# Performance work log

Measured on AMD Instinct MI355X. Metric: run time of the kernel, lower is better.

Reference implementation:

```python
import jax, jax.numpy as jnp
import numpy as np

STRIDES = (8, 16, 32)
C = 80          # num_classes
KA = 3          # anchors per level
TOPK = 100      # per-level top-k
CONF_TH = 0.001
NMS_TH = 0.5
INPUT_SIZE = 2048
ANCHOR_SIZES = np.array([[[10, 13], [16, 30], [33, 23]],
                         [[30, 61], [62, 45], [59, 119]],
                         [[116, 90], [156, 198], [373, 326]]], dtype=np.float32)


def make_anchors(level):
    # Mirrors YOLOv3.create_grid: torch.meshgrid default is 'ij' indexing.
    fmp = INPUT_SIZE // STRIDES[level]
    gy, gx = np.meshgrid(np.arange(fmp), np.arange(fmp), indexing='ij')
    grid_xy = np.stack([gx, gy], axis=-1).reshape(-1, 1, 2).astype(np.float32)  # [HW,1,2]
    grid_xy = np.broadcast_to(grid_xy, (fmp * fmp, KA, 2))
    wh = np.broadcast_to(ANCHOR_SIZES[level][None], (fmp * fmp, KA, 2))
    return jnp.asarray(np.concatenate([grid_xy, wh], axis=-1).reshape(-1, 4))  # [HW*KA,4]


def setup_inputs() -> dict:
    key = jax.random.key(0)
    ks = jax.random.split(key, 9)
    d = {}
    for lvl in range(3):
        N = (INPUT_SIZE // STRIDES[lvl]) ** 2 * KA
        d[f"conf_pred_{lvl + 1}"] = jax.random.normal(ks[3 * lvl], (N, 1), jnp.float32)
        d[f"cls_pred_{lvl + 1}"] = jax.random.normal(ks[3 * lvl + 1], (N, C), jnp.float32)
        d[f"reg_pred_{lvl + 1}"] = jax.random.normal(ks[3 * lvl + 2], (N, 4), jnp.float32) * 0.5
        d[f"anchors_{lvl + 1}"] = make_anchors(lvl)
    return d


def _level(conf, cls, reg, anchors, stride):
    # scores = sigmoid(objectness) * softmax(class logits), flattened over (anchor, class)
    prob = jax.nn.sigmoid(conf) * jax.nn.softmax(cls, axis=-1)      # [N,C]
    scores, idx = jax.lax.top_k(prob.reshape(-1), TOPK)             # [TOPK]
    valid = scores > CONF_TH
    a_idx = idx // C
    labels = idx % C
    r = reg[a_idx]                                                  # [TOPK,4]
    a = anchors[a_idx]                                              # [TOPK,4]
    # decode_boxes: xy = (sigmoid(txy)+grid)*stride ; wh = exp(twh)*anchor_wh
    xy = (jax.nn.sigmoid(r[:, :2]) + a[:, :2]) * stride
    wh = jnp.exp(r[:, 2:]) * a[:, 2:]
    boxes = jnp.concatenate([xy - 0.5 * wh, xy + 0.5 * wh], axis=-1)  # x1y1x2y2
    return scores, labels, boxes, valid


def reference(conf_pred_1, cls_pred_1, reg_pred_1,
              conf_pred_2, cls_pred_2, reg_pred_2,
              conf_pred_3, cls_pred_3, reg_pred_3,
              anchors_1, anchors_2, anchors_3):
    levels = [(conf_pred_1, cls_pred_1, reg_pred_1, anchors_1, STRIDES[0]),
              (conf_pred_2, cls_pred_2, reg_pred_2, anchors_2, STRIDES[1]),
              (conf_pred_3, cls_pred_3, reg_pred_3, anchors_3, STRIDES[2])]
    parts = [_level(*lv) for lv in levels]
    scores = jnp.concatenate([p[0] for p in parts])   # [3*TOPK]
    labels = jnp.concatenate([p[1] for p in parts])
    boxes = jnp.concatenate([p[2] for p in parts], axis=0)
    valid = jnp.concatenate([p[3] for p in parts])

    # Sort all candidates by score descending (greedy NMS order)
    order = jnp.argsort(-scores)
    scores, labels, boxes, valid = scores[order], labels[order], boxes[order], valid[order]

    x1, y1, x2, y2 = boxes[:, 0], boxes[:, 1], boxes[:, 2], boxes[:, 3]
    areas = (x2 - x1) * (y2 - y1)
    xx1 = jnp.maximum(x1[:, None], x1[None, :])
    yy1 = jnp.maximum(y1[:, None], y1[None, :])
    xx2 = jnp.minimum(x2[:, None], x2[None, :])
    yy2 = jnp.minimum(y2[:, None], y2[None, :])
    w = jnp.maximum(1e-10, xx2 - xx1)
    h = jnp.maximum(1e-10, yy2 - yy1)
    inter = w * h
    iou = inter / (areas[:, None] + areas[None, :] - inter)

    K = scores.shape[0]
    idxr = jnp.arange(K)
    # class-wise suppression: only same-label, lower-scored boxes can be suppressed
    sup_cond = (iou > NMS_TH) & (labels[:, None] == labels[None, :]) & (idxr[None, :] > idxr[:, None])

    def body(i, keep):
        return keep & ~(sup_cond[i] & keep[i])

    keep = jax.lax.fori_loop(0, K, body, valid)

    boxes_n = jnp.clip(boxes / INPUT_SIZE, 0.0, 1.0)
    out = jnp.concatenate([boxes_n, scores[:, None], labels.astype(jnp.float32)[:, None]], axis=1)
    return jnp.where(keep[:, None], out, 0.0)   # [3*TOPK, 6] = (x1,y1,x2,y2,score,label)
```

## Files before the change

### kernel.cpp

```cpp
#include <hip/hip_runtime.h>
#include <math.h>
#include <stdint.h>

#define NBUCKET 4096
#define NCOPY   8
#define CAP     16384
#define QCAP    4096
#define STAGE   4096
#define FCAP    1024
#define TOPK    100
#define NLVL    3
#define NCLS    80

#define PA_G1 1024
#define PA_G2 256
#define PA_G3 64
#define CK_G1 192
#define CK_G2 48
#define CK_G3 12

__global__ void zero_kernel(uint4* __restrict__ p)
{
    p[blockIdx.x * 256 + threadIdx.x] = make_uint4(0u, 0u, 0u, 0u);
}

__global__ void passA_kernel(const float* __restrict__ conf1, const float* __restrict__ cls1,
                             const float* __restrict__ conf2, const float* __restrict__ cls2,
                             const float* __restrict__ conf3, const float* __restrict__ cls3,
                             int n1, int n2, int n3,
                             unsigned int* __restrict__ ghist,
                             float* __restrict__ amax)
{
    const float* conf; const float* cls; int nA, nb, b;
    unsigned int* gh; float* am;
    if (blockIdx.x < PA_G1) {
        b = blockIdx.x; conf = conf1; cls = cls1; nA = n1; nb = PA_G1;
        gh = ghist; am = amax;
    } else if (blockIdx.x < PA_G1 + PA_G2) {
        b = blockIdx.x - PA_G1; conf = conf2; cls = cls2; nA = n2; nb = PA_G2;
        gh = ghist + NCOPY * NBUCKET; am = amax + n1;
    } else {
        b = blockIdx.x - PA_G1 - PA_G2; conf = conf3; cls = cls3; nA = n3; nb = PA_G3;
        gh = ghist + 2 * NCOPY * NBUCKET; am = amax + n1 + n2;
    }

    __shared__ unsigned int sh[NBUCKET];
    for (int i = threadIdx.x; i < NBUCKET; i += 256) sh[i] = 0;
    __syncthreads();

    int sub = threadIdx.x & 15;
    int g16 = threadIdx.x >> 4;
    int nChunk = nA >> 4;
    for (int ch = b; ch < nChunk; ch += nb) {
        int a = (ch << 4) + g16;
        float cv  = conf[a];
        float sig = 1.0f / (1.0f + expf(-cv));
        const float* row = cls + (size_t)a * NCLS + sub;
        float c0 = row[0], c1 = row[16], c2 = row[32], c3 = row[48], c4 = row[64];
        float m = fmaxf(fmaxf(fmaxf(c0, c1), fmaxf(c2, c3)), c4);
#pragma unroll
        for (int o = 8; o >= 1; o >>= 1) m = fmaxf(m, __shfl_xor(m, o, 16));
        float s = ((expf(c0 - m) + expf(c1 - m)) + (expf(c2 - m) + expf(c3 - m))) + expf(c4 - m);
#pragma unroll
        for (int o = 8; o >= 1; o >>= 1) s += __shfl_xor(s, o, 16);
        float inv = sig / s;
        if (sub == 0) {
            am[a] = inv;
            unsigned bk = __float_as_uint(inv) >> 18;
            if (bk > NBUCKET - 1) bk = NBUCKET - 1;
            atomicAdd(&sh[bk], 1u);
        }
    }
    __syncthreads();
    unsigned int* g = gh + (b & (NCOPY - 1)) * NBUCKET;
    for (int i = threadIdx.x; i < NBUCKET; i += 256) {
        unsigned v = sh[i];
        if (v) atomicAdd(&g[i], v);
    }
}

__global__ void scan_kernel(const unsigned int* __restrict__ ghist,
                            unsigned int* __restrict__ thresh,
                            unsigned int* __restrict__ ccount)
{
    int lvl = blockIdx.x;
    const unsigned int* h0 = ghist + lvl * NCOPY * NBUCKET;
    __shared__ unsigned int h[NBUCKET];
    __shared__ unsigned int ps[256];
    int t = threadIdx.x;
    if (t == 0) ccount[lvl] = 0;
    for (int bb = t; bb < NBUCKET; bb += 256) {
        unsigned s = 0;
        for (int c = 0; c < NCOPY; c++) s += h0[c * NBUCKET + bb];
        h[bb] = s;
    }
    __syncthreads();
    unsigned cs = 0;
#pragma unroll
    for (int i = 0; i < 16; i++) cs += h[NBUCKET - 1 - (t * 16 + i)];
    ps[t] = cs;
    __syncthreads();
    for (int o = 1; o < 256; o <<= 1) {
        unsigned v = (t >= o) ? ps[t - o] : 0u;
        __syncthreads();
        ps[t] += v;
        __syncthreads();
    }
    unsigned incl = ps[t], excl = incl - cs;
    if (excl < TOPK && incl >= TOPK) {
        unsigned cum = excl, B = 0;
        for (int i = 0; i < 16; i++) {
            int bb = NBUCKET - 1 - (t * 16 + i);
            cum += h[bb];
            if (cum >= TOPK) { B = (unsigned)bb; break; }
        }
        thresh[lvl] = B << 18;
    }
}

__global__ void compact_kernel(const float* __restrict__ conf1, const float* __restrict__ cls1,
                               const float* __restrict__ conf2, const float* __restrict__ cls2,
                               const float* __restrict__ conf3, const float* __restrict__ cls3,
                               int n1, int n2, int n3,
                               const unsigned int* __restrict__ thresh,
                               const float* __restrict__ amax,
                               unsigned int* __restrict__ ccount,
                               float* __restrict__ cscore,
                               unsigned int* __restrict__ cidx)
{
    const float* conf; const float* cls; int bl, lvl; const float* am;
    if (blockIdx.x < CK_G1)              { lvl = 0; bl = blockIdx.x;               conf = conf1; cls = cls1; am = amax; }
    else if (blockIdx.x < CK_G1 + CK_G2) { lvl = 1; bl = blockIdx.x - CK_G1;       conf = conf2; cls = cls2; am = amax + n1; }
    else                                 { lvl = 2; bl = blockIdx.x - CK_G1 - CK_G2; conf = conf3; cls = cls3; am = amax + n1 + n2; }

    __shared__ int qn;
    __shared__ int queue[QCAP];
    if (threadIdx.x == 0) qn = 0;
    __syncthreads();

    unsigned T = thresh[lvl];
    int idx4 = bl * 256 + threadIdx.x;
    const float4* am4 = (const float4*)am;
    float4 v = am4[idx4];
    float vv[4] = {v.x, v.y, v.z, v.w};
#pragma unroll
    for (int j = 0; j < 4; j++) {
        if (__float_as_uint(vv[j]) >= T) {
            int p = atomicAdd(&qn, 1);
            if (p < QCAP) queue[p] = idx4 * 4 + j;
        }
    }
    __syncthreads();
    int qcnt = min(qn, QCAP);
    int grp = threadIdx.x >> 4;
    int sub = threadIdx.x & 15;
    float*        csl = cscore + lvl * CAP;
    unsigned int* cil = cidx   + lvl * CAP;
    for (int q = grp; q < qcnt; q += 16) {
        int a = queue[q];
        float cv  = conf[a];
        float sig = 1.0f / (1.0f + expf(-cv));
        const float* row = cls + (size_t)a * NCLS + sub;
        float c0 = row[0], c1 = row[16], c2 = row[32], c3 = row[48], c4 = row[64];
        float m = fmaxf(fmaxf(fmaxf(c0, c1), fmaxf(c2, c3)), c4);
#pragma unroll
        for (int o = 8; o >= 1; o >>= 1) m = fmaxf(m, __shfl_xor(m, o, 16));
        float e0 = expf(c0 - m), e1 = expf(c1 - m), e2 = expf(c2 - m),
              e3 = expf(c3 - m), e4 = expf(c4 - m);
        float s = ((e0 + e1) + (e2 + e3)) + e4;
#pragma unroll
        for (int o = 8; o >= 1; o >>= 1) s += __shfl_xor(s, o, 16);
        float inv = sig / s;
        float e[5] = {e0, e1, e2, e3, e4};
#pragma unroll
        for (int k = 0; k < 5; k++) {
            float p = e[k] * inv;
            if (e[k] == 1.0f || __float_as_uint(p) >= T) {
                unsigned pos = atomicAdd(&ccount[lvl], 1u);
                if (pos < CAP) {
                    csl[pos] = p;
                    cil[pos] = (unsigned)(a * NCLS + sub + 16 * k);
                }
            }
        }
    }
}

__global__ __launch_bounds__(1024, 4) void select_kernel(
    const float* __restrict__ cscore, const unsigned int* __restrict__ cidx,
    const unsigned int* __restrict__ ccount,
    const unsigned int* __restrict__ thresh,
    float* __restrict__ sel_sc, int* __restrict__ sel_ix)
{
    int lvl = blockIdx.x;
    int tid = threadIdx.x;
    __shared__ float        q_sc[STAGE];
    __shared__ unsigned int q_ix[STAGE];
    __shared__ unsigned int subh[4096];
    __shared__ unsigned int ps[1024];
    __shared__ unsigned int kthr_s;
    __shared__ int          fcnt;
    __shared__ float        f_sc[FCAP];
    __shared__ unsigned int f_ix[FCAP];

    int cnt = min((int)ccount[lvl], CAP);
    const float*        sc = cscore + lvl * CAP;
    const unsigned int* ix = cidx   + lvl * CAP;
    int n = min(cnt, STAGE);
    unsigned B12 = (thresh[lvl] >> 18) << 12;

    for (int i = tid; i < 4096; i += 1024) subh[i] = 0;
    if (tid == 0) fcnt = 0;
    for (int c = tid; c < n; c += 1024) { q_sc[c] = sc[c]; q_ix[c] = ix[c]; }
    if (tid < TOPK) { sel_sc[lvl * TOPK + tid] = -1e30f; sel_ix[lvl * TOPK + tid] = 0; }
    __syncthreads();

    for (int c = tid; c < cnt; c += 1024) {
        float v = (c < n) ? q_sc[c] : sc[c];
        unsigned rel = (__float_as_uint(v) >> 6) - B12;
        if (rel > 4095u) rel = 4095u;
        atomicAdd(&subh[rel], 1u);
    }
    __syncthreads();

    unsigned cs = 0;
#pragma unroll
    for (int i = 0; i < 4; i++) cs += subh[4095 - 4 * tid - i];
    ps[tid] = cs;
    __syncthreads();
    for (int o = 1; o < 1024; o <<= 1) {
        unsigned v = (tid >= o) ? ps[tid - o] : 0u;
        __syncthreads();
        ps[tid] += v;
        __syncthreads();
    }
    {
        unsigned incl = ps[tid], excl = incl - cs;
        if (excl < TOPK && incl >= TOPK) {
            unsigned cum = excl;
            for (int i = 0; i < 4; i++) {
                int sb = 4095 - 4 * tid - i;
                cum += subh[sb];
                if (cum >= TOPK) { kthr_s = (B12 + (unsigned)sb) << 6; break; }
            }
        }
    }
    __syncthreads();
    unsigned kthr = kthr_s;

    for (int c = tid; c < cnt; c += 1024) {
        float v; unsigned vi;
        if (c < n) { v = q_sc[c]; vi = q_ix[c]; }
        else       { v = sc[c];   vi = ix[c];   }
        if (__float_as_uint(v) >= kthr) {
            int p = atomicAdd(&fcnt, 1);
            if (p < FCAP) { f_sc[p] = v; f_ix[p] = vi; }
        }
    }
    __syncthreads();
    int fn = min(fcnt, FCAP);

    for (int c = tid; c < fn; c += 1024) {
        float    my  = f_sc[c];
        unsigned myi = f_ix[c];
        int rank = 0;
        for (int k = 0; k < fn; k++) {
            float v = f_sc[k];
            rank += (v > my) || (v == my && f_ix[k] < myi);
        }
        if (rank < TOPK) {
            sel_sc[lvl * TOPK + rank] = my;
            sel_ix[lvl * TOPK + rank] = (int)myi;
        }
    }
}

__device__ __forceinline__ float rlf(float x, int l)
{
    return __uint_as_float((unsigned)__builtin_amdgcn_readlane((int)__float_as_uint(x), l));
}
__device__ __forceinline__ int rli(int x, int l)
{
    return __builtin_amdgcn_readlane(x, l);
}
__device__ __forceinline__ unsigned long long rl64(unsigned long long x, int b)
{
    unsigned lo = (unsigned)__builtin_amdgcn_readlane((int)(unsigned)x, b);
    unsigned hi = (unsigned)__builtin_amdgcn_readlane((int)(unsigned)(x >> 32), b);
    return ((unsigned long long)hi << 32) | lo;
}

__global__ void prep_kernel(
    const float* __restrict__ reg1, const float* __restrict__ anch1,
    const float* __restrict__ reg2, const float* __restrict__ anch2,
    const float* __restrict__ reg3, const float* __restrict__ anch3,
    const float* __restrict__ sel_sc, const int* __restrict__ sel_ix,
    float* __restrict__ t_score, float* __restrict__ t_box,
    int* __restrict__ t_label, int* __restrict__ t_valid)
{
    int tid  = threadIdx.x;
    int lane = tid & 63;

    float sg[5];
#pragma unroll
    for (int g = 0; g < 5; g++) {
        int k = g * 64 + lane;
        sg[g] = (k < 300) ? sel_sc[k] : -INFINITY;
    }

    float my = (tid < 300) ? sel_sc[tid] : -INFINITY;
    int rank = 0;
#pragma unroll
    for (int g = 0; g < 5; g++) {
        int base = g * 64;
#pragma unroll 1
        for (int ii = 0; ii < 64; ii++) {
            float v = rlf(sg[g], ii);
            int k = base + ii;
            rank += (v > my) || (v == my && k < tid);
        }
    }

    if (tid < 300) {
        int lvl = tid / TOPK;
        const float* reg = lvl == 0 ? reg1 : (lvl == 1 ? reg2 : reg3);
        const float* anc = lvl == 0 ? anch1 : (lvl == 1 ? anch2 : anch3);
        float stride = lvl == 0 ? 8.0f : (lvl == 1 ? 16.0f : 32.0f);
        int  idx = sel_ix[tid];
        int a   = idx / NCLS;
        int lab = idx % NCLS;
        float r0 = reg[4 * a + 0], r1 = reg[4 * a + 1], r2 = reg[4 * a + 2], r3 = reg[4 * a + 3];
        float a0 = anc[4 * a + 0], a1 = anc[4 * a + 1], a2 = anc[4 * a + 2], a3 = anc[4 * a + 3];
        float cx = (1.0f / (1.0f + expf(-r0)) + a0) * stride;
        float cy = (1.0f / (1.0f + expf(-r1)) + a1) * stride;
        float w  = expf(r2) * a2;
        float h  = expf(r3) * a3;
        t_score[rank]       = my;
        t_box[4 * rank + 0] = cx - 0.5f * w;
        t_box[4 * rank + 1] = cy - 0.5f * h;
        t_box[4 * rank + 2] = cx + 0.5f * w;
        t_box[4 * rank + 3] = cy + 0.5f * h;
        t_label[rank] = lab;
        t_valid[rank] = my > 0.001f;
    }
}

__global__ void sup_kernel(const float* __restrict__ t_box,
                           const int* __restrict__ t_label,
                           unsigned long long* __restrict__ sup_ws)
{
    int tid  = threadIdx.x;
    int lane = tid & 63;
    int w    = tid >> 6;
    int rbase = 20 * blockIdx.x;

    float bx1 = 0, by1 = 0, bx2 = 0, by2 = 0, areaj = 0;
    int labj = -1;
    if (tid < 300) {
        bx1 = t_box[4 * tid + 0]; by1 = t_box[4 * tid + 1];
        bx2 = t_box[4 * tid + 2]; by2 = t_box[4 * tid + 3];
        labj = t_label[tid];
        areaj = (bx2 - bx1) * (by2 - by1);
    }

    float rx1 = 0, ry1 = 0, rx2 = 0, ry2 = 0, rar = 1.0f;
    int rlab = -9;
    int r = rbase + lane;
    if (lane < 20 && r < 300) {
        rx1 = t_box[4 * r + 0]; ry1 = t_box[4 * r + 1];
        rx2 = t_box[4 * r + 2]; ry2 = t_box[4 * r + 3];
        rar = (rx2 - rx1) * (ry2 - ry1);
        rlab = t_label[r];
    }

#pragma unroll 1
    for (int ii = 0; ii < 20; ii++) {
        int i = rbase + ii;
        float xi1 = rlf(rx1, ii), yi1 = rlf(ry1, ii);
        float xi2 = rlf(rx2, ii), yi2 = rlf(ry2, ii);
        float ari = rlf(rar, ii);
        int  labi = rli(rlab, ii);
        float xx1 = fmaxf(xi1, bx1), yy1 = fmaxf(yi1, by1);
        float xx2 = fminf(xi2, bx2), yy2 = fminf(yi2, by2);
        float ww = fmaxf(1e-10f, xx2 - xx1);
        float hh = fmaxf(1e-10f, yy2 - yy1);
        float inter = ww * hh;
        float iou = inter / (ari + areaj - inter);
        bool p = (tid > i) && (labj == labi) && (iou > 0.5f) && (tid < 300);
        unsigned long long m = __ballot(p);
        if (lane == 0) sup_ws[i * 5 + w] = m;
    }
}

__global__ void nmsfin_kernel(const float* __restrict__ t_score,
                              const float* __restrict__ t_box,
                              const int* __restrict__ t_label,
                              const int* __restrict__ t_valid,
                              const unsigned long long* __restrict__ sup_ws,
                              float* __restrict__ out)
{
    int lane = threadIdx.x;

    unsigned long long s0[5], s1[5], s2[5], s3[5], s4[5];
#pragma unroll
    for (int q = 0; q < 5; q++) {
        s0[q] = sup_ws[(lane)       * 5 + q];
        s1[q] = sup_ws[(lane + 64)  * 5 + q];
        s2[q] = sup_ws[(lane + 128) * 5 + q];
        s3[q] = sup_ws[(lane + 192) * 5 + q];
        s4[q] = (lane + 256 < 300) ? sup_ws[(lane + 256) * 5 + q] : 0ull;
    }

    unsigned long long k0 = __ballot(t_valid[lane] != 0);
    unsigned long long k1 = __ballot(t_valid[lane + 64] != 0);
    unsigned long long k2 = __ballot(t_valid[lane + 128] != 0);
    unsigned long long k3 = __ballot(t_valid[lane + 192] != 0);
    unsigned long long k4 = __ballot((lane + 256 < 300) ? (t_valid[lane + 256] != 0) : false);

    unsigned long long nz0 = __ballot((s0[0] | s0[1] | s0[2] | s0[3] | s0[4]) != 0ull);
    unsigned long long nz1 = __ballot((s1[0] | s1[1] | s1[2] | s1[3] | s1[4]) != 0ull);
    unsigned long long nz2 = __ballot((s2[0] | s2[1] | s2[2] | s2[3] | s2[4]) != 0ull);
    unsigned long long nz3 = __ballot((s3[0] | s3[1] | s3[2] | s3[3] | s3[4]) != 0ull);
    unsigned long long nz4 = __ballot((s4[0] | s4[1] | s4[2] | s4[3] | s4[4]) != 0ull);

#define NMS_SPARSE(SR, KR, NZ)                                                \
    {                                                                         \
        unsigned long long m = (NZ);                                          \
        while (m) {                                                           \
            int b = __builtin_ctzll(m);                                       \
            m &= m - 1ull;                                                    \
            if ((KR >> b) & 1ull) {                                           \
                k0 &= ~rl64(SR[0], b);                                        \
                k1 &= ~rl64(SR[1], b);                                        \
                k2 &= ~rl64(SR[2], b);                                        \
                k3 &= ~rl64(SR[3], b);                                        \
                k4 &= ~rl64(SR[4], b);                                        \
            }                                                                 \
        }                                                                     \
    }
    NMS_SPARSE(s0, k0, nz0)
    NMS_SPARSE(s1, k1, nz1)
    NMS_SPARSE(s2, k2, nz2)
    NMS_SPARSE(s3, k3, nz3)
    NMS_SPARSE(s4, k4, nz4)
#undef NMS_SPARSE

#pragma unroll 1
    for (int e = lane; e < 300 * 6; e += 64) {
        int row = e / 6, col = e % 6;
        unsigned long long kw = (row < 64) ? k0 : (row < 128) ? k1 : (row < 192) ? k2
                              : (row < 256) ? k3 : k4;
        bool kept = (kw >> (row & 63)) & 1ull;
        float v = 0.0f;
        if (kept) {
            if (col < 4) {
                v = t_box[4 * row + col] * (1.0f / 2048.0f);
                v = fminf(fmaxf(v, 0.0f), 1.0f);
            } else if (col == 4) {
                v = t_score[row];
            } else {
                v = (float)t_label[row];
            }
        }
        out[e] = v;
    }
}

extern "C" void kernel_launch(void* const* d_in, const int* in_sizes, int n_in,
                              void* d_out, int out_size, void* d_ws, size_t ws_size,
                              hipStream_t stream)
{
    const float* conf1 = (const float*)d_in[0];
    const float* cls1  = (const float*)d_in[1];
    const float* reg1  = (const float*)d_in[2];
    const float* anch1 = (const float*)d_in[3];
    const float* conf2 = (const float*)d_in[4];
    const float* cls2  = (const float*)d_in[5];
    const float* reg2  = (const float*)d_in[6];
    const float* anch2 = (const float*)d_in[7];
    const float* conf3 = (const float*)d_in[8];
    const float* cls3  = (const float*)d_in[9];
    const float* reg3  = (const float*)d_in[10];
    const float* anch3 = (const float*)d_in[11];

    int N1 = in_sizes[0];
    int N2 = in_sizes[4];
    int N3 = in_sizes[8];

    unsigned int* wsu    = (unsigned int*)d_ws;
    unsigned int* hist   = wsu;
    unsigned int* thresh = wsu + NLVL * NCOPY * NBUCKET;
    unsigned int* ccount = thresh + NLVL;
    float*        amax   = (float*)(wsu + NLVL * NCOPY * NBUCKET + 16);
    float*        cscore = amax + (N1 + N2 + N3);
    unsigned int* cidx   = (unsigned int*)(cscore + NLVL * CAP);
    float*        sel_sc = (float*)(cidx + NLVL * CAP);
    int*          sel_ix = (int*)(sel_sc + NLVL * TOPK);
    float*        t_score = (float*)(sel_ix + NLVL * TOPK);
    float*        t_box   = t_score + 300;
    int*          t_label = (int*)(t_box + 1200);
    int*          t_valid = t_label + 300;
    unsigned long long* sup_ws =
        (unsigned long long*)(((uintptr_t)(t_valid + 300) + 15) & ~(uintptr_t)15);

    zero_kernel<<<96, 256, 0, stream>>>((uint4*)hist);

    passA_kernel<<<PA_G1 + PA_G2 + PA_G3, 256, 0, stream>>>(
        conf1, cls1, conf2, cls2, conf3, cls3, N1, N2, N3, hist, amax);

    scan_kernel<<<NLVL, 256, 0, stream>>>(hist, thresh, ccount);

    compact_kernel<<<CK_G1 + CK_G2 + CK_G3, 256, 0, stream>>>(
        conf1, cls1, conf2, cls2, conf3, cls3, N1, N2, N3,
        thresh, amax, ccount, cscore, cidx);

    select_kernel<<<NLVL, 1024, 0, stream>>>(cscore, cidx, ccount, thresh, sel_sc, sel_ix);

    prep_kernel<<<1, 320, 0, stream>>>(reg1, anch1, reg2, anch2, reg3, anch3,
                                       sel_sc, sel_ix, t_score, t_box, t_label, t_valid);

    sup_kernel<<<15, 320, 0, stream>>>(t_box, t_label, sup_ws);

    nmsfin_kernel<<<1, 64, 0, stream>>>(t_score, t_box, t_label, t_valid, sup_ws, (float*)d_out);
}
```

Baseline: 92.55 us.

## Fuse tail kernels via last-block-done counters and unroll passA two chunks per iteration

Merges select with prep, and sup with the NMS finalize, into two kernels. Each uses an atomic completion counter so that the last block to finish runs the follow-on stage, which removes two kernel launches and their inter-kernel gaps. The select block size drops from 1024 to 320 threads, and the block-wide prefix scan becomes a single-wavefront shuffle scan over 64-bucket groups. passA now processes two chunks per loop iteration to get more loads in flight. The counters are zeroed in zero_kernel, which adds threadfence and atomic synchronisation overhead, and fewer threads now share the select work.

```diff
diff --git a/kernel.cpp b/kernel.cpp
--- a/kernel.cpp
+++ b/kernel.cpp
@@ -19,9 +19,10 @@
 #define CK_G2 48
 #define CK_G3 12
 
-__global__ void zero_kernel(uint4* __restrict__ p)
+__global__ void zero_kernel(uint4* __restrict__ p, unsigned int* __restrict__ ctr)
 {
     p[blockIdx.x * 256 + threadIdx.x] = make_uint4(0u, 0u, 0u, 0u);
+    if (blockIdx.x == 0 && threadIdx.x == 0) { ctr[0] = 0u; ctr[1] = 0u; }
 }
 
 __global__ void passA_kernel(const float* __restrict__ conf1, const float* __restrict__ cls1,
@@ -51,24 +52,52 @@
     int sub = threadIdx.x & 15;
     int g16 = threadIdx.x >> 4;
     int nChunk = nA >> 4;
-    for (int ch = b; ch < nChunk; ch += nb) {
-        int a = (ch << 4) + g16;
-        float cv  = conf[a];
-        float sig = 1.0f / (1.0f + expf(-cv));
-        const float* row = cls + (size_t)a * NCLS + sub;
-        float c0 = row[0], c1 = row[16], c2 = row[32], c3 = row[48], c4 = row[64];
-        float m = fmaxf(fmaxf(fmaxf(c0, c1), fmaxf(c2, c3)), c4);
-#pragma unroll
-        for (int o = 8; o >= 1; o >>= 1) m = fmaxf(m, __shfl_xor(m, o, 16));
-        float s = ((expf(c0 - m) + expf(c1 - m)) + (expf(c2 - m) + expf(c3 - m))) + expf(c4 - m);
-#pragma unroll
-        for (int o = 8; o >= 1; o >>= 1) s += __shfl_xor(s, o, 16);
-        float inv = sig / s;
-        if (sub == 0) {
-            am[a] = inv;
-            unsigned bk = __float_as_uint(inv) >> 18;
-            if (bk > NBUCKET - 1) bk = NBUCKET - 1;
-            atomicAdd(&sh[bk], 1u);
+    for (int ch = b; ch < nChunk; ch += 2 * nb) {
+        int a0 = (ch << 4) + g16;
+        int ch1 = ch + nb;
+        bool has1 = ch1 < nChunk;
+        float cv0 = conf[a0];
+        const float* r0 = cls + (size_t)a0 * NCLS + sub;
+        float A0 = r0[0], A1 = r0[16], A2 = r0[32], A3 = r0[48], A4 = r0[64];
+        float cv1 = 0.0f, B0 = 0, B1 = 0, B2 = 0, B3 = 0, B4 = 0;
+        int a1 = 0;
+        if (has1) {
+            a1 = (ch1 << 4) + g16;
+            cv1 = conf[a1];
+            const float* r1 = cls + (size_t)a1 * NCLS + sub;
+            B0 = r1[0]; B1 = r1[16]; B2 = r1[32]; B3 = r1[48]; B4 = r1[64];
+        }
+        {
+            float sig = 1.0f / (1.0f + expf(-cv0));
+            float m = fmaxf(fmaxf(fmaxf(A0, A1), fmaxf(A2, A3)), A4);
+#pragma unroll
+            for (int o = 8; o >= 1; o >>= 1) m = fmaxf(m, __shfl_xor(m, o, 16));
+            float s = ((expf(A0 - m) + expf(A1 - m)) + (expf(A2 - m) + expf(A3 - m))) + expf(A4 - m);
+#pragma unroll
+            for (int o = 8; o >= 1; o >>= 1) s += __shfl_xor(s, o, 16);
+            float inv = sig / s;
+            if (sub == 0) {
+                am[a0] = inv;
+                unsigned bk = __float_as_uint(inv) >> 18;
+                if (bk > NBUCKET - 1) bk = NBUCKET - 1;
+                atomicAdd(&sh[bk], 1u);
+            }
+        }
+        if (has1) {
+            float sig = 1.0f / (1.0f + expf(-cv1));
+            float m = fmaxf(fmaxf(fmaxf(B0, B1), fmaxf(B2, B3)), B4);
+#pragma unroll
+            for (int o = 8; o >= 1; o >>= 1) m = fmaxf(m, __shfl_xor(m, o, 16));
+            float s = ((expf(B0 - m) + expf(B1 - m)) + (expf(B2 - m) + expf(B3 - m))) + expf(B4 - m);
+#pragma unroll
+            for (int o = 8; o >= 1; o >>= 1) s += __shfl_xor(s, o, 16);
+            float inv = sig / s;
+            if (sub == 0) {
+                am[a1] = inv;
+                unsigned bk = __float_as_uint(inv) >> 18;
+                if (bk > NBUCKET - 1) bk = NBUCKET - 1;
+                atomicAdd(&sh[bk], 1u);
+            }
         }
     }
     __syncthreads();
@@ -186,22 +215,43 @@
     }
 }
 
-__global__ __launch_bounds__(1024, 4) void select_kernel(
+__device__ __forceinline__ float rlf(float x, int l)
+{
+    return __uint_as_float((unsigned)__builtin_amdgcn_readlane((int)__float_as_uint(x), l));
+}
+__device__ __forceinline__ int rli(int x, int l)
+{
+    return __builtin_amdgcn_readlane(x, l);
+}
+__device__ __forceinline__ unsigned long long rl64(unsigned long long x, int b)
+{
+    unsigned lo = (unsigned)__builtin_amdgcn_readlane((int)(unsigned)x, b);
+    unsigned hi = (unsigned)__builtin_amdgcn_readlane((int)(unsigned)(x >> 32), b);
+    return ((unsigned long long)hi << 32) | lo;
+}
+
+__global__ __launch_bounds__(320) void select_prep_kernel(
     const float* __restrict__ cscore, const unsigned int* __restrict__ cidx,
     const unsigned int* __restrict__ ccount,
     const unsigned int* __restrict__ thresh,
-    float* __restrict__ sel_sc, int* __restrict__ sel_ix)
+    float* __restrict__ sel_sc, int* __restrict__ sel_ix,
+    const float* __restrict__ reg1, const float* __restrict__ anch1,
+    const float* __restrict__ reg2, const float* __restrict__ anch2,
+    const float* __restrict__ reg3, const float* __restrict__ anch3,
+    float* __restrict__ t_score, float* __restrict__ t_box,
+    int* __restrict__ t_label, int* __restrict__ t_valid,
+    unsigned int* __restrict__ sel_done)
 {
     int lvl = blockIdx.x;
     int tid = threadIdx.x;
     __shared__ float        q_sc[STAGE];
     __shared__ unsigned int q_ix[STAGE];
     __shared__ unsigned int subh[4096];
-    __shared__ unsigned int ps[1024];
     __shared__ unsigned int kthr_s;
     __shared__ int          fcnt;
     __shared__ float        f_sc[FCAP];
     __shared__ unsigned int f_ix[FCAP];
+    __shared__ int          lastflag;
 
     int cnt = min((int)ccount[lvl], CAP);
     const float*        sc = cscore + lvl * CAP;
@@ -209,13 +259,13 @@
     int n = min(cnt, STAGE);
     unsigned B12 = (thresh[lvl] >> 18) << 12;
 
-    for (int i = tid; i < 4096; i += 1024) subh[i] = 0;
+    for (int i = tid; i < 4096; i += 320) subh[i] = 0;
     if (tid == 0) fcnt = 0;
-    for (int c = tid; c < n; c += 1024) { q_sc[c] = sc[c]; q_ix[c] = ix[c]; }
+    for (int c = tid; c < n; c += 320) { q_sc[c] = sc[c]; q_ix[c] = ix[c]; }
     if (tid < TOPK) { sel_sc[lvl * TOPK + tid] = -1e30f; sel_ix[lvl * TOPK + tid] = 0; }
     __syncthreads();
 
-    for (int c = tid; c < cnt; c += 1024) {
+    for (int c = tid; c < cnt; c += 320) {
         float v = (c < n) ? q_sc[c] : sc[c];
         unsigned rel = (__float_as_uint(v) >> 6) - B12;
         if (rel > 4095u) rel = 4095u;
@@ -223,32 +273,29 @@
     }
     __syncthreads();
 
-    unsigned cs = 0;
-#pragma unroll
-    for (int i = 0; i < 4; i++) cs += subh[4095 - 4 * tid - i];
-    ps[tid] = cs;
-    __syncthreads();
-    for (int o = 1; o < 1024; o <<= 1) {
-        unsigned v = (tid >= o) ? ps[tid - o] : 0u;
-        __syncthreads();
-        ps[tid] += v;
-        __syncthreads();
-    }
-    {
-        unsigned incl = ps[tid], excl = incl - cs;
-        if (excl < TOPK && incl >= TOPK) {
+    if (tid < 64) {
+        int base = 4095 - (tid << 6);
+        unsigned csum = 0;
+        for (int i = 0; i < 64; i++) csum += subh[base - i];
+        unsigned v = csum;
+        for (int o = 1; o < 64; o <<= 1) {
+            unsigned u = __shfl_up(v, o);
+            if (tid >= o) v += u;
+        }
+        unsigned excl = v - csum;
+        if (excl < TOPK && v >= TOPK) {
             unsigned cum = excl;
-            for (int i = 0; i < 4; i++) {
-                int sb = 4095 - 4 * tid - i;
-                cum += subh[sb];
-                if (cum >= TOPK) { kthr_s = (B12 + (unsigned)sb) << 6; break; }
+            for (int i = 0; i < 64; i++) {
+                int bb = base - i;
+                cum += subh[bb];
+                if (cum >= TOPK) { kthr_s = (B12 + (unsigned)bb) << 6; break; }
             }
         }
     }
     __syncthreads();
     unsigned kthr = kthr_s;
 
-    for (int c = tid; c < cnt; c += 1024) {
+    for (int c = tid; c < cnt; c += 320) {
         float v; unsigned vi;
         if (c < n) { v = q_sc[c]; vi = q_ix[c]; }
         else       { v = sc[c];   vi = ix[c];   }
@@ -260,7 +307,7 @@
     __syncthreads();
     int fn = min(fcnt, FCAP);
 
-    for (int c = tid; c < fn; c += 1024) {
+    for (int c = tid; c < fn; c += 320) {
         float    my  = f_sc[c];
         unsigned myi = f_ix[c];
         int rank = 0;
@@ -273,86 +320,75 @@
             sel_ix[lvl * TOPK + rank] = (int)myi;
         }
     }
-}
-
-__device__ __forceinline__ float rlf(float x, int l)
-{
-    return __uint_as_float((unsigned)__builtin_amdgcn_readlane((int)__float_as_uint(x), l));
-}
-__device__ __forceinline__ int rli(int x, int l)
-{
-    return __builtin_amdgcn_readlane(x, l);
-}
-__device__ __forceinline__ unsigned long long rl64(unsigned long long x, int b)
-{
-    unsigned lo = (unsigned)__builtin_amdgcn_readlane((int)(unsigned)x, b);
-    unsigned hi = (unsigned)__builtin_amdgcn_readlane((int)(unsigned)(x >> 32), b);
-    return ((unsigned long long)hi << 32) | lo;
-}
-
-__global__ void prep_kernel(
-    const float* __restrict__ reg1, const float* __restrict__ anch1,
-    const float* __restrict__ reg2, const float* __restrict__ anch2,
-    const float* __restrict__ reg3, const float* __restrict__ anch3,
-    const float* __restrict__ sel_sc, const int* __restrict__ sel_ix,
-    float* __restrict__ t_score, float* __restrict__ t_box,
-    int* __restrict__ t_label, int* __restrict__ t_valid)
-{
-    int tid  = threadIdx.x;
-    int lane = tid & 63;
-
-    float sg[5];
-#pragma unroll
-    for (int g = 0; g < 5; g++) {
-        int k = g * 64 + lane;
-        sg[g] = (k < 300) ? sel_sc[k] : -INFINITY;
-    }
-
-    float my = (tid < 300) ? sel_sc[tid] : -INFINITY;
-    int rank = 0;
-#pragma unroll
-    for (int g = 0; g < 5; g++) {
-        int base = g * 64;
+
+    __syncthreads();
+    if (tid == 0) {
+        __threadfence();
+        unsigned prev = atomicAdd(sel_done, 1u);
+        lastflag = (prev == NLVL - 1);
+    }
+    __syncthreads();
+    if (!lastflag) return;
+    if (tid == 0) __threadfence();
+    __syncthreads();
+
+    {
+        int lane = tid & 63;
+        float sg[5];
+#pragma unroll
+        for (int g = 0; g < 5; g++) {
+            int k = g * 64 + lane;
+            sg[g] = (k < 300) ? sel_sc[k] : -INFINITY;
+        }
+        float my = (tid < 300) ? sel_sc[tid] : -INFINITY;
+        int rank = 0;
+#pragma unroll
+        for (int g = 0; g < 5; g++) {
+            int base = g * 64;
 #pragma unroll 1
-        for (int ii = 0; ii < 64; ii++) {
-            float v = rlf(sg[g], ii);
-            int k = base + ii;
-            rank += (v > my) || (v == my && k < tid);
-        }
-    }
-
-    if (tid < 300) {
-        int lvl = tid / TOPK;
-        const float* reg = lvl == 0 ? reg1 : (lvl == 1 ? reg2 : reg3);
-        const float* anc = lvl == 0 ? anch1 : (lvl == 1 ? anch2 : anch3);
-        float stride = lvl == 0 ? 8.0f : (lvl == 1 ? 16.0f : 32.0f);
-        int  idx = sel_ix[tid];
-        int a   = idx / NCLS;
-        int lab = idx % NCLS;
-        float r0 = reg[4 * a + 0], r1 = reg[4 * a + 1], r2 = reg[4 * a + 2], r3 = reg[4 * a + 3];
-        float a0 = anc[4 * a + 0], a1 = anc[4 * a + 1], a2 = anc[4 * a + 2], a3 = anc[4 * a + 3];
-        float cx = (1.0f / (1.0f + expf(-r0)) + a0) * stride;
-        float cy = (1.0f / (1.0f + expf(-r1)) + a1) * stride;
-        float w  = expf(r2) * a2;
-        float h  = expf(r3) * a3;
-        t_score[rank]       = my;
-        t_box[4 * rank + 0] = cx - 0.5f * w;
-        t_box[4 * rank + 1] = cy - 0.5f * h;
-        t_box[4 * rank + 2] = cx + 0.5f * w;
-        t_box[4 * rank + 3] = cy + 0.5f * h;
-        t_label[rank] = lab;
-        t_valid[rank] = my > 0.001f;
-    }
-}
-
-__global__ void sup_kernel(const float* __restrict__ t_box,
-                           const int* __restrict__ t_label,
-                           unsigned long long* __restrict__ sup_ws)
+            for (int ii = 0; ii < 64; ii++) {
+                float v = rlf(sg[g], ii);
+                int k = base + ii;
+                rank += (v > my) || (v == my && k < tid);
+            }
+        }
+        if (tid < 300) {
+            int lv = tid / TOPK;
+            const float* reg = lv == 0 ? reg1 : (lv == 1 ? reg2 : reg3);
+            const float* anc = lv == 0 ? anch1 : (lv == 1 ? anch2 : anch3);
+            float stride = lv == 0 ? 8.0f : (lv == 1 ? 16.0f : 32.0f);
+            int  idx = sel_ix[tid];
+            int a   = idx / NCLS;
+            int lab = idx % NCLS;
+            float r0 = reg[4 * a + 0], r1 = reg[4 * a + 1], r2 = reg[4 * a + 2], r3 = reg[4 * a + 3];
+            float a0 = anc[4 * a + 0], a1 = anc[4 * a + 1], a2 = anc[4 * a + 2], a3 = anc[4 * a + 3];
+            float cx = (1.0f / (1.0f + expf(-r0)) + a0) * stride;
+            float cy = (1.0f / (1.0f + expf(-r1)) + a1) * stride;
+            float w  = expf(r2) * a2;
+            float h  = expf(r3) * a3;
+            t_score[rank]       = my;
+            t_box[4 * rank + 0] = cx - 0.5f * w;
+            t_box[4 * rank + 1] = cy - 0.5f * h;
+            t_box[4 * rank + 2] = cx + 0.5f * w;
+            t_box[4 * rank + 3] = cy + 0.5f * h;
+            t_label[rank] = lab;
+            t_valid[rank] = my > 0.001f;
+        }
+    }
+}
+
+__global__ __launch_bounds__(320) void supnms_kernel(
+    const float* __restrict__ t_score, const float* __restrict__ t_box,
+    const int* __restrict__ t_label, const int* __restrict__ t_valid,
+    unsigned long long* __restrict__ sup_ws,
+    unsigned int* __restrict__ sup_done,
+    float* __restrict__ out)
 {
     int tid  = threadIdx.x;
     int lane = tid & 63;
     int w    = tid >> 6;
     int rbase = 20 * blockIdx.x;
+    __shared__ int lastflag;
 
     float bx1 = 0, by1 = 0, bx2 = 0, by2 = 0, areaj = 0;
     int labj = -1;
@@ -390,79 +426,82 @@
         unsigned long long m = __ballot(p);
         if (lane == 0) sup_ws[i * 5 + w] = m;
     }
-}
-
-__global__ void nmsfin_kernel(const float* __restrict__ t_score,
-                              const float* __restrict__ t_box,
-                              const int* __restrict__ t_label,
-                              const int* __restrict__ t_valid,
-                              const unsigned long long* __restrict__ sup_ws,
-                              float* __restrict__ out)
-{
-    int lane = threadIdx.x;
-
-    unsigned long long s0[5], s1[5], s2[5], s3[5], s4[5];
-#pragma unroll
-    for (int q = 0; q < 5; q++) {
-        s0[q] = sup_ws[(lane)       * 5 + q];
-        s1[q] = sup_ws[(lane + 64)  * 5 + q];
-        s2[q] = sup_ws[(lane + 128) * 5 + q];
-        s3[q] = sup_ws[(lane + 192) * 5 + q];
-        s4[q] = (lane + 256 < 300) ? sup_ws[(lane + 256) * 5 + q] : 0ull;
-    }
-
-    unsigned long long k0 = __ballot(t_valid[lane] != 0);
-    unsigned long long k1 = __ballot(t_valid[lane + 64] != 0);
-    unsigned long long k2 = __ballot(t_valid[lane + 128] != 0);
-    unsigned long long k3 = __ballot(t_valid[lane + 192] != 0);
-    unsigned long long k4 = __ballot((lane + 256 < 300) ? (t_valid[lane + 256] != 0) : false);
-
-    unsigned long long nz0 = __ballot((s0[0] | s0[1] | s0[2] | s0[3] | s0[4]) != 0ull);
-    unsigned long long nz1 = __ballot((s1[0] | s1[1] | s1[2] | s1[3] | s1[4]) != 0ull);
-    unsigned long long nz2 = __ballot((s2[0] | s2[1] | s2[2] | s2[3] | s2[4]) != 0ull);
-    unsigned long long nz3 = __ballot((s3[0] | s3[1] | s3[2] | s3[3] | s3[4]) != 0ull);
-    unsigned long long nz4 = __ballot((s4[0] | s4[1] | s4[2] | s4[3] | s4[4]) != 0ull);
+
+    __syncthreads();
+    if (tid == 0) {
+        __threadfence();
+        unsigned prev = atomicAdd(sup_done, 1u);
+        lastflag = (prev == 14);
+    }
+    __syncthreads();
+    if (!lastflag) return;
+    if (tid == 0) __threadfence();
+    __syncthreads();
+
+    if (tid < 64) {
+        unsigned long long s0[5], s1[5], s2[5], s3[5], s4[5];
+#pragma unroll
+        for (int q = 0; q < 5; q++) {
+            s0[q] = sup_ws[(lane)       * 5 + q];
+            s1[q] = sup_ws[(lane + 64)  * 5 + q];
+            s2[q] = sup_ws[(lane + 128) * 5 + q];
+            s3[q] = sup_ws[(lane + 192) * 5 + q];
+            s4[q] = (lane + 256 < 300) ? sup_ws[(lane + 256) * 5 + q] : 0ull;
+        }
+
+        unsigned long long k0 = __ballot(t_valid[lane] != 0);
+        unsigned long long k1 = __ballot(t_valid[lane + 64] != 0);
+        unsigned long long k2 = __ballot(t_valid[lane + 128] != 0);
+        unsigned long long k3 = __ballot(t_valid[lane + 192] != 0);
+        unsigned long long k4 = __ballot((lane + 256 < 300) ? (t_valid[lane + 256] != 0) : false);
+
+        unsigned long long nz0 = __ballot((s0[0] | s0[1] | s0[2] | s0[3] | s0[4]) != 0ull);
+        unsigned long long nz1 = __ballot((s1[0] | s1[1] | s1[2] | s1[3] | s1[4]) != 0ull);
+        unsigned long long nz2 = __ballot((s2[0] | s2[1] | s2[2] | s2[3] | s2[4]) != 0ull);
+        unsigned long long nz3 = __ballot((s3[0] | s3[1] | s3[2] | s3[3] | s3[4]) != 0ull);
+        unsigned long long nz4 = __ballot((s4[0] | s4[1] | s4[2] | s4[3] | s4[4]) != 0ull);
 
 #define NMS_SPARSE(SR, KR, NZ)                                                \
-    {                                                                         \
-        unsigned long long m = (NZ);                                          \
-        while (m) {                                                           \
-            int b = __builtin_ctzll(m);                                       \
-            m &= m - 1ull;                                                    \
-            if ((KR >> b) & 1ull) {                                           \
-                k0 &= ~rl64(SR[0], b);                                        \
-                k1 &= ~rl64(SR[1], b);                                        \
-                k2 &= ~rl64(SR[2], b);                                        \
-                k3 &= ~rl64(SR[3], b);                                        \
-                k4 &= ~rl64(SR[4], b);                                        \
+        {                                                                     \
+            unsigned long long m = (NZ);                                      \
+            while (m) {                                                       \
+                int b = __builtin_ctzll(m);                                   \
+                m &= m - 1ull;                                                \
+                if ((KR >> b) & 1ull) {                                       \
+                    k0 &= ~rl64(SR[0], b);                                    \
+                    k1 &= ~rl64(SR[1], b);                                    \
+                    k2 &= ~rl64(SR[2], b);                                    \
+                    k3 &= ~rl64(SR[3], b);                                    \
+                    k4 &= ~rl64(SR[4], b);                                    \
+                }                                                             \
             }                                                                 \
-        }                                                                     \
-    }
-    NMS_SPARSE(s0, k0, nz0)
-    NMS_SPARSE(s1, k1, nz1)
-    NMS_SPARSE(s2, k2, nz2)
-    NMS_SPARSE(s3, k3, nz3)
-    NMS_SPARSE(s4, k4, nz4)
+        }
+        NMS_SPARSE(s0, k0, nz0)
+        NMS_SPARSE(s1, k1, nz1)
+        NMS_SPARSE(s2, k2, nz2)
+        NMS_SPARSE(s3, k3, nz3)
+        NMS_SPARSE(s4, k4, nz4)
 #undef NMS_SPARSE
 
 #pragma unroll 1
-    for (int e = lane; e < 300 * 6; e += 64) {
-        int row = e / 6, col = e % 6;
-        unsigned long long kw = (row < 64) ? k0 : (row < 128) ? k1 : (row < 192) ? k2
-                              : (row < 256) ? k3 : k4;
-        bool kept = (kw >> (row & 63)) & 1ull;
-        float v = 0.0f;
-        if (kept) {
-            if (col < 4) {
-                v = t_box[4 * row + col] * (1.0f / 2048.0f);
-                v = fminf(fmaxf(v, 0.0f), 1.0f);
-            } else if (col == 4) {
-                v = t_score[row];
-            } else {
-                v = (float)t_label[row];
+        for (int e = lane; e < 300 * 6; e += 64) {
+            int row = e / 6, col = e % 6;
+            unsigned long long kw = (row < 64) ? k0 : (row < 128) ? k1 : (row < 192) ? k2
+                                  : (row < 256) ? k3 : k4;
+            bool kept = (kw >> (row & 63)) & 1ull;
+            float v = 0.0f;
+            if (kept) {
+                if (col < 4) {
+                    v = t_box[4 * row + col] * (1.0f / 2048.0f);
+                    v = fminf(fmaxf(v, 0.0f), 1.0f);
+                } else if (col == 4) {
+                    v = t_score[row];
+                } else {
+                    v = (float)t_label[row];
+                }
             }
-        }
-        out[e] = v;
+            out[e] = v;
+        }
     }
 }
 
@@ -491,6 +530,7 @@
     unsigned int* hist   = wsu;
     unsigned int* thresh = wsu + NLVL * NCOPY * NBUCKET;
     unsigned int* ccount = thresh + NLVL;
+    unsigned int* ctrs   = thresh + 6;
     float*        amax   = (float*)(wsu + NLVL * NCOPY * NBUCKET + 16);
     float*        cscore = amax + (N1 + N2 + N3);
     unsigned int* cidx   = (unsigned int*)(cscore + NLVL * CAP);
@@ -503,7 +543,7 @@
     unsigned long long* sup_ws =
         (unsigned long long*)(((uintptr_t)(t_valid + 300) + 15) & ~(uintptr_t)15);
 
-    zero_kernel<<<96, 256, 0, stream>>>((uint4*)hist);
+    zero_kernel<<<96, 256, 0, stream>>>((uint4*)hist, ctrs);
 
     passA_kernel<<<PA_G1 + PA_G2 + PA_G3, 256, 0, stream>>>(
         conf1, cls1, conf2, cls2, conf3, cls3, N1, N2, N3, hist, amax);
@@ -514,12 +554,11 @@
         conf1, cls1, conf2, cls2, conf3, cls3, N1, N2, N3,
         thresh, amax, ccount, cscore, cidx);
 
-    select_kernel<<<NLVL, 1024, 0, stream>>>(cscore, cidx, ccount, thresh, sel_sc, sel_ix);
-
-    prep_kernel<<<1, 320, 0, stream>>>(reg1, anch1, reg2, anch2, reg3, anch3,
-                                       sel_sc, sel_ix, t_score, t_box, t_label, t_valid);
-
-    sup_kernel<<<15, 320, 0, stream>>>(t_box, t_label, sup_ws);
-
-    nmsfin_kernel<<<1, 64, 0, stream>>>(t_score, t_box, t_label, t_valid, sup_ws, (float*)d_out);
-}
+    select_prep_kernel<<<NLVL, 320, 0, stream>>>(
+        cscore, cidx, ccount, thresh, sel_sc, sel_ix,
+        reg1, anch1, reg2, anch2, reg3, anch3,
+        t_score, t_box, t_label, t_valid, &ctrs[0]);
+
+    supnms_kernel<<<15, 320, 0, stream>>>(
+        t_score, t_box, t_label, t_valid, sup_ws, &ctrs[1], (float*)d_out);
+}
```

Measured after the change: 95.14 us. 1.03x slower.
